# Performance work log

Hardware: AMD Instinct MI355X
Metric: run time of the kernel (lower is better)

Reference implementation:

```python
import jax, jax.numpy as jnp
import numpy as np

N = 10000      # nodes
E = 160000     # edges
B = 16         # graphs in batch
F_NODE = 42
F_EDGE = 12
D = 256        # hidden_dim
H = 4          # heads
C = D // H     # per-head channels = 64
L = 5          # num_layers
NEG_SLOPE = 0.2  # GATConv leaky_relu slope


def layernorm(x, g, b, eps=1e-5):
    mu = jnp.mean(x, axis=-1, keepdims=True)
    var = jnp.var(x, axis=-1, keepdims=True)
    return (x - mu) * jax.lax.rsqrt(var + eps) * g + b


def setup_inputs() -> dict:
    key = jax.random.key(0)
    ks = jax.random.split(key, 20)
    def w(i, shape, scale=0.05):
        return jax.random.normal(ks[i], shape, dtype=jnp.float32) * scale
    return {
        "x": jax.random.normal(ks[0], (N, F_NODE), dtype=jnp.float32),
        "edge_attr": jax.random.normal(ks[1], (E, F_EDGE), dtype=jnp.float32),
        "edge_index": jax.random.randint(ks[2], (2, E), 0, N),
        "batch": jnp.sort(jax.random.randint(ks[3], (N,), 0, B)),
        # node / edge encoders
        "enc_w": w(4, (F_NODE, D)), "enc_b": jnp.zeros((D,), jnp.float32),
        "eenc_w": w(5, (F_EDGE, D)), "eenc_b": jnp.zeros((D,), jnp.float32),
        # stacked GAT layer params [L, ...]
        "gat_w": w(6, (L, D, D)),          # lin_src == lin_dst (shared in PyG for Tensor input)
        "att_src": w(7, (L, H, C)),
        "att_dst": w(8, (L, H, C)),
        "att_edge": w(9, (L, H, C)),
        "gat_ew": w(10, (L, D, D)),        # lin_edge
        "gat_b": jnp.zeros((L, D), jnp.float32),
        "ln_g": jnp.ones((L, D), jnp.float32),
        "ln_b": jnp.zeros((L, D), jnp.float32),
        # attention pooling gate MLP
        "gate_w1": w(11, (D, D)), "gate_b1": jnp.zeros((D,), jnp.float32),
        "gate_w2": w(12, (D, 1)), "gate_b2": jnp.zeros((1,), jnp.float32),
        # MLP readout (mlp_layers=2)
        "ro_w1": w(13, (D, D)), "ro_b1": jnp.zeros((D,), jnp.float32),
        "ro_w2": w(14, (D, D)), "ro_b2": jnp.zeros((D,), jnp.float32),
    }


def reference(x, edge_index, edge_attr, batch, enc_w, enc_b, eenc_w, eenc_b,
              gat_w, att_src, att_dst, att_edge, gat_ew, gat_b, ln_g, ln_b,
              gate_w1, gate_b1, gate_w2, gate_b2, ro_w1, ro_b1, ro_w2, ro_b2):
    src0, dst0 = edge_index[0], edge_index[1]

    # encoders (dropout is identity at eval)
    h = jax.nn.relu(x @ enc_w + enc_b)                      # [N, D]
    e = jax.nn.relu(edge_attr @ eenc_w + eenc_b)            # [E, D]

    # GATConv add_self_loops with fill_value='mean': self-loop edge feature is
    # the mean of incoming edge features per destination node.
    esum = jax.ops.segment_sum(e, dst0, num_segments=N)
    cnt = jax.ops.segment_sum(jnp.ones((E,), e.dtype), dst0, num_segments=N)
    e_self = esum / jnp.maximum(cnt, 1.0)[:, None]
    e_full = jnp.concatenate([e, e_self], axis=0)           # [E+N, D]
    loops = jnp.arange(N)
    src = jnp.concatenate([src0, loops])
    dst = jnp.concatenate([dst0, loops])

    for l in range(L):
        xh = (h @ gat_w[l]).reshape(N, H, C)                # [N, H, C]
        a_s = jnp.einsum('nhc,hc->nh', xh, att_src[l])      # [N, H]
        a_d = jnp.einsum('nhc,hc->nh', xh, att_dst[l])
        eh = (e_full @ gat_ew[l]).reshape(-1, H, C)         # [E+N, H, C]
        a_e = jnp.einsum('ehc,hc->eh', eh, att_edge[l])
        alpha = jax.nn.leaky_relu(a_s[src] + a_d[dst] + a_e, NEG_SLOPE)  # [E+N, H]
        # softmax over incoming edges per destination node (stable)
        m = jax.lax.stop_gradient(jax.ops.segment_max(alpha, dst, num_segments=N))
        ex = jnp.exp(alpha - m[dst])
        den = jax.ops.segment_sum(ex, dst, num_segments=N)
        attn = ex / den[dst]                                # [E+N, H]
        msg = xh[src] * attn[:, :, None]                    # [E+N, H, C]
        out = jax.ops.segment_sum(msg, dst, num_segments=N).reshape(N, D) + gat_b[l]
        out = jax.nn.relu(layernorm(out, ln_g[l], ln_b[l]))
        h = h + out                                         # residual

    # GlobalAttention pooling: softmax(gate_nn(h)) per graph, weighted sum
    gate = (jax.nn.relu(h @ gate_w1 + gate_b1) @ gate_w2 + gate_b2)[:, 0]  # [N]
    gm = jax.lax.stop_gradient(jax.ops.segment_max(gate, batch, num_segments=B))
    ge = jnp.exp(gate - gm[batch])
    gd = jax.ops.segment_sum(ge, batch, num_segments=B)
    wgt = ge / gd[batch]
    g_embed = jax.ops.segment_sum(h * wgt[:, None], batch, num_segments=B)  # [B, D]

    # MLP readout
    return jax.nn.relu(g_embed @ ro_w1 + ro_b1) @ ro_w2 + ro_b2  # [B, D]
```

## Files before the change

kernel.cpp:

```cpp
#include <hip/hip_runtime.h>
#include <math.h>

#define DD 256
#define HH 4
#define CC 64
#define LL 5
#define NEG_SLOPE 0.2f
#define LH 20
#define WCAP 192

typedef __bf16 bf16x8 __attribute__((ext_vector_type(8)));
typedef __bf16 bf16x4 __attribute__((ext_vector_type(4)));
typedef float f32x4 __attribute__((ext_vector_type(4)));

static __device__ __forceinline__ float lrelu(float x) {
    return x > 0.0f ? x : NEG_SLOPE * x;
}

__global__ __launch_bounds__(256) void mega_setup_kernel(
    const float* __restrict__ gat_ew, const float* __restrict__ att_edge,
    float* __restrict__ wproj,
    const float* __restrict__ gat_w, const float* __restrict__ gate_w1,
    __bf16* __restrict__ wf,
    const int* __restrict__ dst_arr, int* __restrict__ deg,
    const float* __restrict__ x, const float* __restrict__ enc_w,
    const float* __restrict__ enc_b, float* __restrict__ h,
    __bf16* __restrict__ hbf,
    float* __restrict__ g_embed, float* __restrict__ gate_out,
    int N, int E, int B) {
    int blk = blockIdx.x;
    int tid = threadIdx.x;
    int EB = (E + 255) >> 8;
    if (blk < 5) {
        int l = blk;
        int k = tid;
        const float* W = gat_ew + (size_t)l * DD * DD;
        const float* att = att_edge + l * DD;
        for (int hh = 0; hh < HH; ++hh) {
            float s = 0.f;
            #pragma unroll
            for (int c = 0; c < CC; ++c)
                s += W[k * DD + hh * CC + c] * att[hh * CC + c];
            wproj[k * LH + l * HH + hh] = s;
        }
        return;
    }
    blk -= 5;
    if (blk < 192) {
        int b = blk;
        int l = b >> 5;
        int rem = b & 31;
        int y = rem >> 3, ks = rem & 7;
        int t = tid >> 6, lane = tid & 63;
        int q = lane >> 4, r15 = lane & 15;
        const float* W = (l < 5) ? (gat_w + (size_t)l * DD * DD) : gate_w1;
        size_t obase = (((size_t)b * 4 + t) * 64 + lane) * 8;
        int kbase = ks * 32 + q * 8;
        int col = y * 64 + t * 16 + r15;
        #pragma unroll
        for (int j = 0; j < 8; ++j)
            wf[obase + j] = (__bf16)W[(size_t)(kbase + j) * DD + col];
        return;
    }
    blk -= 192;
    if (blk < EB) {
        int e = blk * 256 + tid;
        if (e < E) atomicAdd(&deg[dst_arr[e]], 1);
        return;
    }
    blk -= EB;
    if (blk < N) {
        int n = blk;
        __shared__ float xs[42];
        if (tid < 42) xs[tid] = x[(size_t)n * 42 + tid];
        __syncthreads();
        float acc = enc_b[tid];
        #pragma unroll
        for (int f = 0; f < 42; ++f) acc += xs[f] * enc_w[f * DD + tid];
        float v = fmaxf(acc, 0.f);
        h[(size_t)n * DD + tid] = v;
        hbf[(size_t)n * DD + tid] = (__bf16)v;
        return;
    }
    blk -= N;
    if (blk == 0) {
        for (int i = tid; i < B * DD; i += 256) g_embed[i] = 0.f;
        return;
    }
    for (int i = tid; i < N; i += 256) gate_out[i] = 0.f;
}

__global__ __launch_bounds__(1024) void scan_pack_kernel(
    const int* __restrict__ deg, int* __restrict__ row_ptr,
    int* __restrict__ cursor, int n,
    const float* __restrict__ eenc_w, const float* __restrict__ eenc_b,
    const float* __restrict__ wproj, __bf16* __restrict__ wfe,
    __bf16* __restrict__ wfp) {
    int tid = threadIdx.x;
    if (blockIdx.x == 1) {
        {
            int idx = tid;
            int t = idx >> 6, lane = idx & 63;
            int q = lane >> 4, r15 = lane & 15;
            int col = t * 16 + r15;
            #pragma unroll
            for (int j = 0; j < 8; ++j) {
                int k = q * 8 + j;
                float v = (k < 12) ? eenc_w[k * 256 + col]
                                   : (k == 12 ? eenc_b[col] : 0.f);
                wfe[(size_t)idx * 8 + j] = (__bf16)v;
            }
        }
        {
            int idx = tid;
            int sidx = idx >> 6, lane = idx & 63;
            int s = sidx >> 1, t2 = sidx & 1;
            int q = lane >> 4, r15 = lane & 15;
            int col = t2 * 16 + r15;
            #pragma unroll
            for (int j = 0; j < 8; ++j) {
                int k = s * 32 + q * 8 + j;
                float v = (col < LH) ? wproj[k * LH + col] : 0.f;
                wfp[(size_t)idx * 8 + j] = (__bf16)v;
            }
        }
        return;
    }
    __shared__ int wsum[16];
    __shared__ int carry_s;
    int w = tid >> 6, lane = tid & 63;
    if (tid == 0) carry_s = 0;
    __syncthreads();
    for (int base = 0; base < n; base += 1024) {
        int i = base + tid;
        int v = (i < n) ? deg[i] : 0;
        int carry = carry_s;
        int s = v;
        #pragma unroll
        for (int off = 1; off < 64; off <<= 1) {
            int t = __shfl_up(s, off, 64);
            if (lane >= off) s += t;
        }
        if (lane == 63) wsum[w] = s;
        __syncthreads();
        if (w == 0 && lane < 16) {
            int ws = wsum[lane];
            #pragma unroll
            for (int off = 1; off < 16; off <<= 1) {
                int t = __shfl_up(ws, off, 64);
                if (lane >= off) ws += t;
            }
            wsum[lane] = ws;
        }
        __syncthreads();
        int waveoff = (w == 0) ? 0 : wsum[w - 1];
        if (i < n) {
            int ex = carry + waveoff + s - v;
            row_ptr[i] = ex;
            cursor[i] = ex;
        }
        __syncthreads();
        if (tid == 0) carry_s = carry + wsum[15];
        __syncthreads();
    }
    if (tid == 0) row_ptr[n] = carry_s;
}

__global__ __launch_bounds__(256) void edge_mfma_kernel(
    const float* __restrict__ edge_attr, const __bf16* __restrict__ wfe,
    const __bf16* __restrict__ wfp,
    const int* __restrict__ src_arr, const int* __restrict__ dst_arr,
    int* __restrict__ cursor, int* __restrict__ csr_src,
    float* __restrict__ a_e, int E, int N) {
    __shared__ __bf16 sm[4][16][264];
    __shared__ int pkbuf[4][16];
    int tid = threadIdx.x;
    int w = tid >> 6, lane = tid & 63;
    int q = lane >> 4, r15 = lane & 15;
    int eb = blockIdx.x * 64 + w * 16;
    int e = eb + r15;
    int ec = min(e, E - 1);
    if (q == 0 && e < E) {
        int d = dst_arr[e];
        int pk = atomicAdd(&cursor[d], 1);
        csr_src[pk] = src_arr[e];
        pkbuf[w][r15] = pk;
    }
    bf16x8 a1;
    #pragma unroll
    for (int j = 0; j < 8; ++j) a1[j] = (__bf16)0.f;
    if (q == 0) {
        const float4* p = (const float4*)(edge_attr + (size_t)ec * 12);
        float4 p0 = p[0], p1 = p[1];
        a1[0] = (__bf16)p0.x; a1[1] = (__bf16)p0.y; a1[2] = (__bf16)p0.z; a1[3] = (__bf16)p0.w;
        a1[4] = (__bf16)p1.x; a1[5] = (__bf16)p1.y; a1[6] = (__bf16)p1.z; a1[7] = (__bf16)p1.w;
    } else if (q == 1) {
        float4 p2 = *(const float4*)(edge_attr + (size_t)ec * 12 + 8);
        a1[0] = (__bf16)p2.x; a1[1] = (__bf16)p2.y; a1[2] = (__bf16)p2.z; a1[3] = (__bf16)p2.w;
        a1[4] = (__bf16)1.0f;
    }
    const bf16x8* wfeP = (const bf16x8*)wfe;
    f32x4 zero = (f32x4){0.f, 0.f, 0.f, 0.f};
    #pragma unroll
    for (int t = 0; t < 16; ++t) {
        bf16x8 bfr = wfeP[t * 64 + lane];
        f32x4 c = __builtin_amdgcn_mfma_f32_16x16x32_bf16(a1, bfr, zero, 0, 0, 0);
        int col = t * 16 + r15;
        #pragma unroll
        for (int r = 0; r < 4; ++r)
            sm[w][q * 4 + r][col] = (__bf16)fmaxf(c[r], 0.f);
    }
    const bf16x8* wfpP = (const bf16x8*)wfp;
    f32x4 c2[2];
    c2[0] = zero; c2[1] = zero;
    #pragma unroll
    for (int s = 0; s < 8; ++s) {
        bf16x8 a2 = *(const bf16x8*)&sm[w][r15][s * 32 + q * 8];
        #pragma unroll
        for (int t2 = 0; t2 < 2; ++t2)
            c2[t2] = __builtin_amdgcn_mfma_f32_16x16x32_bf16(
                a2, wfpP[(s * 2 + t2) * 64 + lane], c2[t2], 0, 0, 0);
    }
    size_t stride_l = (size_t)(E + N) * 4;
    #pragma unroll
    for (int t2 = 0; t2 < 2; ++t2) {
        int col = t2 * 16 + r15;
        if (col >= LH) continue;
        int l = col >> 2, hh = col & 3;
        #pragma unroll
        for (int r = 0; r < 4; ++r) {
            int e2 = eb + q * 4 + r;
            if (e2 < E) {
                int pk = pkbuf[w][q * 4 + r];
                a_e[(size_t)l * stride_l + (size_t)pk * 4 + hh] = c2[t2][r];
            }
        }
    }
}

__global__ void self_ae_kernel(const int* __restrict__ row_ptr,
                               float* __restrict__ a_e, int N, int E) {
    int i = blockIdx.x * 256 + threadIdx.x;
    if (i >= N * LH) return;
    int n = i / LH;
    int j = i % LH;
    int l = j >> 2, hh = j & 3;
    int rs = row_ptr[n], re = row_ptr[n + 1];
    size_t base = (size_t)l * (size_t)(E + N) * 4;
    float s = 0.f;
    for (int k = rs; k < re; ++k)
        s += a_e[base + (size_t)k * 4 + hh];
    a_e[base + (size_t)(E + n) * 4 + hh] = s / (float)max(re - rs, 1);
}

__global__ __launch_bounds__(256) void gemm_mfma_kernel(
    const __bf16* __restrict__ hbf, const __bf16* __restrict__ wf,
    __bf16* __restrict__ xhbf, int M,
    const float* __restrict__ att_src, const float* __restrict__ att_dst,
    float* __restrict__ a_s, float* __restrict__ a_d,
    const float* __restrict__ bias, const float* __restrict__ gate_w2,
    const float* __restrict__ gate_b2, float* __restrict__ gate_out) {
    int tid = threadIdx.x;
    int w = tid >> 6, lane = tid & 63;
    int q = lane >> 4, r15 = lane & 15;
    int m0 = blockIdx.x * 64;
    int y2 = blockIdx.y;
    int arow = m0 + w * 16 + r15;
    int arowc = min(arow, M - 1);
    const __bf16* ap = hbf + (size_t)arowc * DD + q * 8;
    const bf16x8* wfP = (const bf16x8*)wf;
    f32x4 acc[8];
    #pragma unroll
    for (int g = 0; g < 8; ++g) acc[g] = (f32x4){0.f, 0.f, 0.f, 0.f};
    #pragma unroll
    for (int ks = 0; ks < 8; ++ks) {
        bf16x8 a = *(const bf16x8*)(ap + ks * 32);
        #pragma unroll
        for (int g = 0; g < 8; ++g) {
            int y = y2 * 2 + (g >> 2);
            int t = g & 3;
            bf16x8 b = wfP[(size_t)(((y * 8 + ks) * 4) + t) * 64 + lane];
            acc[g] = __builtin_amdgcn_mfma_f32_16x16x32_bf16(a, b, acc[g], 0, 0, 0);
        }
    }
    if (xhbf) {
        #pragma unroll
        for (int g = 0; g < 8; ++g) {
            int col = (y2 * 8 + g) * 16 + r15;
            #pragma unroll
            for (int r = 0; r < 4; ++r) {
                int rc = m0 + w * 16 + q * 4 + r;
                if (rc < M) xhbf[(size_t)rc * DD + col] = (__bf16)acc[g][r];
            }
        }
    }
    if (att_src) {
        #pragma unroll
        for (int r = 0; r < 4; ++r) {
            float ps0 = 0.f, pd0 = 0.f, ps1 = 0.f, pd1 = 0.f;
            #pragma unroll
            for (int g = 0; g < 8; ++g) {
                int col = (y2 * 8 + g) * 16 + r15;
                float v = acc[g][r];
                if (g < 4) { ps0 += v * att_src[col]; pd0 += v * att_dst[col]; }
                else       { ps1 += v * att_src[col]; pd1 += v * att_dst[col]; }
            }
            #pragma unroll
            for (int mask = 1; mask < 16; mask <<= 1) {
                ps0 += __shfl_xor(ps0, mask, 64);
                pd0 += __shfl_xor(pd0, mask, 64);
                ps1 += __shfl_xor(ps1, mask, 64);
                pd1 += __shfl_xor(pd1, mask, 64);
            }
            int rc = m0 + w * 16 + q * 4 + r;
            if (r15 == 0 && rc < M) {
                a_s[rc * HH + y2 * 2 + 0] = ps0;
                a_d[rc * HH + y2 * 2 + 0] = pd0;
                a_s[rc * HH + y2 * 2 + 1] = ps1;
                a_d[rc * HH + y2 * 2 + 1] = pd1;
            }
        }
    }
    if (gate_w2) {
        #pragma unroll
        for (int r = 0; r < 4; ++r) {
            float pg = 0.f;
            #pragma unroll
            for (int g = 0; g < 8; ++g) {
                int col = (y2 * 8 + g) * 16 + r15;
                pg += fmaxf(acc[g][r] + bias[col], 0.f) * gate_w2[col];
            }
            #pragma unroll
            for (int mask = 1; mask < 16; mask <<= 1) pg += __shfl_xor(pg, mask, 64);
            int rc = m0 + w * 16 + q * 4 + r;
            if (r15 == 0 && rc < M) {
                float add = pg + (y2 == 0 ? gate_b2[0] : 0.f);
                atomicAdd(&gate_out[rc], add);
            }
        }
    }
}

__global__ __launch_bounds__(256) void gat_message8_kernel(
    const __bf16* __restrict__ xhbf, const float* __restrict__ a_s,
    const float* __restrict__ a_d, const float* __restrict__ a_e,
    const int* __restrict__ row_ptr, const int* __restrict__ csr_src,
    const float* __restrict__ gat_b,
    const float* __restrict__ ln_g, const float* __restrict__ ln_b,
    float* __restrict__ h, __bf16* __restrict__ hbf, int N, int E) {
    __shared__ float lws[4][WCAP * 4];
    __shared__ int lsrc[4][WCAP];
    int tid = threadIdx.x;
    int w = tid >> 6, lane = tid & 63;
    int n = blockIdx.x * 4 + w;
    if (n >= N) return;
    int hh = lane >> 4, j = lane & 15;
    int rs = row_ptr[n], re = row_ptr[n + 1];
    int deg = re - rs;
    float adn = a_d[n * HH + hh];
    float al_self = lrelu(a_s[n * HH + hh] + adn + a_e[(size_t)(E + n) * 4 + hh]);
    float m = al_self, den = 0.f;
    for (int k = rs + j; k < re; k += 16) {
        int kk = k - rs;
        int s = csr_src[k];
        float a = lrelu(a_s[s * HH + hh] + adn + a_e[(size_t)k * 4 + hh]);
        if (kk < WCAP) {
            lws[w][kk * 4 + hh] = a;
            if (hh == 0) lsrc[w][kk] = s;
        }
        float mn = fmaxf(m, a);
        den = den * __expf(m - mn) + __expf(a - mn);
        m = mn;
    }
    #pragma unroll
    for (int off = 1; off < 16; off <<= 1) {
        float m2 = __shfl_xor(m, off, 64);
        float d2 = __shfl_xor(den, off, 64);
        float mn = fmaxf(m, m2);
        den = den * __expf(m - mn) + d2 * __expf(m2 - mn);
        m = mn;
    }
    den += __expf(al_self - m);
    float inv_den = 1.0f / den;
    int cap = min(deg, WCAP);
    for (int kk = j; kk < cap; kk += 16)
        lws[w][kk * 4 + hh] = __expf(lws[w][kk * 4 + hh] - m) * inv_den;
    float wself = __expf(al_self - m) * inv_den;
    bf16x4 xsb = *((const bf16x4*)(xhbf + (size_t)n * DD) + lane);
    float4 acc;
    acc.x = wself * (float)xsb[0]; acc.y = wself * (float)xsb[1];
    acc.z = wself * (float)xsb[2]; acc.w = wself * (float)xsb[3];
    if (deg <= WCAP) {
        int k = rs;
        for (; k + 3 < re; k += 4) {
            int kk = k - rs;
            int s0 = lsrc[w][kk + 0], s1_ = lsrc[w][kk + 1];
            int s2_ = lsrc[w][kk + 2], s3_ = lsrc[w][kk + 3];
            float w0 = lws[w][(kk + 0) * 4 + hh], w1 = lws[w][(kk + 1) * 4 + hh];
            float w2 = lws[w][(kk + 2) * 4 + hh], w3 = lws[w][(kk + 3) * 4 + hh];
            bf16x4 x0 = *((const bf16x4*)(xhbf + (size_t)s0 * DD) + lane);
            bf16x4 x1 = *((const bf16x4*)(xhbf + (size_t)s1_ * DD) + lane);
            bf16x4 x2 = *((const bf16x4*)(xhbf + (size_t)s2_ * DD) + lane);
            bf16x4 x3 = *((const bf16x4*)(xhbf + (size_t)s3_ * DD) + lane);
            acc.x += w0 * (float)x0[0] + w1 * (float)x1[0] + w2 * (float)x2[0] + w3 * (float)x3[0];
            acc.y += w0 * (float)x0[1] + w1 * (float)x1[1] + w2 * (float)x2[1] + w3 * (float)x3[1];
            acc.z += w0 * (float)x0[2] + w1 * (float)x1[2] + w2 * (float)x2[2] + w3 * (float)x3[2];
            acc.w += w0 * (float)x0[3] + w1 * (float)x1[3] + w2 * (float)x2[3] + w3 * (float)x3[3];
        }
        for (; k < re; ++k) {
            int kk = k - rs;
            int s0 = lsrc[w][kk];
            float w0 = lws[w][kk * 4 + hh];
            bf16x4 x0 = *((const bf16x4*)(xhbf + (size_t)s0 * DD) + lane);
            acc.x += w0 * (float)x0[0]; acc.y += w0 * (float)x0[1];
            acc.z += w0 * (float)x0[2]; acc.w += w0 * (float)x0[3];
        }
    } else {
        for (int k = rs; k < re; ++k) {
            int kk = k - rs;
            int s0;
            float w0;
            if (kk < WCAP) { s0 = lsrc[w][kk]; w0 = lws[w][kk * 4 + hh]; }
            else {
                s0 = csr_src[k];
                w0 = __expf(lrelu(a_s[s0 * HH + hh] + adn + a_e[(size_t)k * 4 + hh]) - m) * inv_den;
            }
            bf16x4 x0 = *((const bf16x4*)(xhbf + (size_t)s0 * DD) + lane);
            acc.x += w0 * (float)x0[0]; acc.y += w0 * (float)x0[1];
            acc.z += w0 * (float)x0[2]; acc.w += w0 * (float)x0[3];
        }
    }
    float4 gb = *((const float4*)gat_b + lane);
    float4 val;
    val.x = acc.x + gb.x; val.y = acc.y + gb.y;
    val.z = acc.z + gb.z; val.w = acc.w + gb.w;
    float s1 = val.x + val.y + val.z + val.w;
    float s2 = val.x * val.x + val.y * val.y + val.z * val.z + val.w * val.w;
    #pragma unroll
    for (int off = 1; off < 64; off <<= 1) {
        s1 += __shfl_xor(s1, off, 64);
        s2 += __shfl_xor(s2, off, 64);
    }
    float mu = s1 * (1.0f / DD);
    float var = s2 * (1.0f / DD) - mu * mu;
    float rstd = rsqrtf(var + 1e-5f);
    float4 lg = *((const float4*)ln_g + lane);
    float4 lb = *((const float4*)ln_b + lane);
    float4 nv;
    nv.x = fmaxf((val.x - mu) * rstd * lg.x + lb.x, 0.f);
    nv.y = fmaxf((val.y - mu) * rstd * lg.y + lb.y, 0.f);
    nv.z = fmaxf((val.z - mu) * rstd * lg.z + lb.z, 0.f);
    nv.w = fmaxf((val.w - mu) * rstd * lg.w + lb.w, 0.f);
    float4* hp = (float4*)(h + (size_t)n * DD) + lane;
    float4 hv = *hp;
    hv.x += nv.x; hv.y += nv.y; hv.z += nv.z; hv.w += nv.w;
    *hp = hv;
    bf16x4 hb;
    hb[0] = (__bf16)hv.x; hb[1] = (__bf16)hv.y;
    hb[2] = (__bf16)hv.z; hb[3] = (__bf16)hv.w;
    *((bf16x4*)(hbf + (size_t)n * DD) + lane) = hb;
}

__global__ __launch_bounds__(256) void gseg_kernel(
    const float* __restrict__ gate, const int* __restrict__ batch,
    float* __restrict__ gmax, float* __restrict__ gden, int N) {
    int b = blockIdx.x;
    int tid = threadIdx.x;
    __shared__ int bounds[2];
    if (tid < 2) {
        int target = b + tid;
        int lo = 0, hi = N;
        while (lo < hi) {
            int mid = (lo + hi) >> 1;
            if (batch[mid] < target) lo = mid + 1; else hi = mid;
        }
        bounds[tid] = lo;
    }
    __syncthreads();
    int s0 = bounds[0], s1 = bounds[1];
    __shared__ float red[256];
    float m = -1e30f;
    for (int i = s0 + tid; i < s1; i += 256) m = fmaxf(m, gate[i]);
    red[tid] = m;
    __syncthreads();
    for (int off = 128; off; off >>= 1) {
        if (tid < off) red[tid] = fmaxf(red[tid], red[tid + off]);
        __syncthreads();
    }
    float gm = red[0];
    __syncthreads();
    float s = 0.f;
    for (int i = s0 + tid; i < s1; i += 256) s += __expf(gate[i] - gm);
    red[tid] = s;
    __syncthreads();
    for (int off = 128; off; off >>= 1) {
        if (tid < off) red[tid] += red[tid + off];
        __syncthreads();
    }
    if (tid == 0) {
        gmax[b] = gm;
        gden[b] = red[0];
    }
}

#define POOL_CHUNK 32
__global__ __launch_bounds__(256) void pool_scatter_kernel(
    const float* __restrict__ h, const float* __restrict__ gate,
    const float* __restrict__ gmax, const float* __restrict__ gden,
    const int* __restrict__ batch, float* __restrict__ g_embed, int N) {
    int i0 = blockIdx.x * POOL_CHUNK;
    int d = threadIdx.x;
    int iend = min(i0 + POOL_CHUNK, N);
    float acc = 0.f;
    int cur = batch[i0];
    for (int i = i0; i < iend; ++i) {
        int b = batch[i];
        if (b != cur) {
            atomicAdd(&g_embed[cur * DD + d], acc);
            acc = 0.f;
            cur = b;
        }
        float wgt = __expf(gate[i] - gmax[b]) / gden[b];
        acc += wgt * h[(size_t)i * DD + d];
    }
    atomicAdd(&g_embed[cur * DD + d], acc);
}

__global__ __launch_bounds__(256) void readout_kernel(
    const float* __restrict__ g_embed, const float* __restrict__ w1,
    const float* __restrict__ b1, const float* __restrict__ w2,
    const float* __restrict__ b2, float* __restrict__ out) {
    int b = blockIdx.x;
    int tid = threadIdx.x;
    __shared__ float gvec[256];
    __shared__ float hid[256];
    gvec[tid] = g_embed[b * DD + tid];
    __syncthreads();
    float hv = b1[tid];
    for (int k = 0; k < DD; ++k) hv += gvec[k] * w1[k * DD + tid];
    hid[tid] = fmaxf(hv, 0.f);
    __syncthreads();
    float o = b2[tid];
    for (int t = 0; t < DD; ++t) o += hid[t] * w2[t * DD + tid];
    out[b * DD + tid] = o;
}

extern "C" void kernel_launch(void* const* d_in, const int* in_sizes, int n_in,
                              void* d_out, int out_size, void* d_ws, size_t ws_size,
                              hipStream_t stream) {
    const float* x        = (const float*)d_in[0];
    const float* edge_attr= (const float*)d_in[1];
    const int*   edge_idx = (const int*)d_in[2];
    const int*   batch    = (const int*)d_in[3];
    const float* enc_w    = (const float*)d_in[4];
    const float* enc_b    = (const float*)d_in[5];
    const float* eenc_w   = (const float*)d_in[6];
    const float* eenc_b   = (const float*)d_in[7];
    const float* gat_w    = (const float*)d_in[8];
    const float* att_src  = (const float*)d_in[9];
    const float* att_dst  = (const float*)d_in[10];
    const float* att_edge = (const float*)d_in[11];
    const float* gat_ew   = (const float*)d_in[12];
    const float* gat_b    = (const float*)d_in[13];
    const float* ln_g     = (const float*)d_in[14];
    const float* ln_b     = (const float*)d_in[15];
    const float* gate_w1  = (const float*)d_in[16];
    const float* gate_b1  = (const float*)d_in[17];
    const float* gate_w2  = (const float*)d_in[18];
    const float* gate_b2  = (const float*)d_in[19];
    const float* ro_w1    = (const float*)d_in[20];
    const float* ro_b1    = (const float*)d_in[21];
    const float* ro_w2    = (const float*)d_in[22];
    const float* ro_b2    = (const float*)d_in[23];
    float* out = (float*)d_out;

    const int N = in_sizes[0] / 42;
    const int E = in_sizes[1] / 12;
    const int B = out_size / DD;

    char* p = (char*)d_ws;
    auto alloc = [&](size_t bytes) {
        char* r = p;
        p += (bytes + 255) & ~(size_t)255;
        return (void*)r;
    };
    float*  h       = (float*)alloc((size_t)N * DD * 4);
    __bf16* hbf     = (__bf16*)alloc((size_t)N * DD * 2);
    __bf16* xhbf    = (__bf16*)alloc((size_t)N * DD * 2);
    float*  a_s     = (float*)alloc((size_t)N * HH * 4);
    float*  a_d     = (float*)alloc((size_t)N * HH * 4);
    float*  a_e_csr = (float*)alloc((size_t)LL * (E + N) * 4 * 4);
    float*  wproj   = (float*)alloc((size_t)DD * LH * 4);
    __bf16* wfe     = (__bf16*)alloc((size_t)16 * 64 * 8 * 2);
    __bf16* wfp     = (__bf16*)alloc((size_t)16 * 64 * 8 * 2);
    __bf16* wf      = (__bf16*)alloc((size_t)6 * DD * DD * 2);
    float*  gate    = (float*)alloc((size_t)N * 4);
    float*  g_embed = (float*)alloc((size_t)B * DD * 4);
    float*  gmax    = (float*)alloc((size_t)B * 4);
    float*  gden    = (float*)alloc((size_t)B * 4);
    int* deg        = (int*)alloc((size_t)N * 4);
    int* row_ptr    = (int*)alloc((size_t)(N + 1) * 4);
    int* cursor     = (int*)alloc((size_t)N * 4);
    int* csr_src    = (int*)alloc((size_t)E * 4);

    const int* src_arr = edge_idx;
    const int* dst_arr = edge_idx + E;

    hipMemsetAsync(deg, 0, (size_t)N * 4, stream);

    const int EB = (E + 255) / 256;
    int mega_grid = 5 + 192 + EB + N + 2;
    mega_setup_kernel<<<mega_grid, 256, 0, stream>>>(
        gat_ew, att_edge, wproj, gat_w, gate_w1, wf,
        dst_arr, deg, x, enc_w, enc_b, h, hbf, g_embed, gate, N, E, B);
    scan_pack_kernel<<<2, 1024, 0, stream>>>(
        deg, row_ptr, cursor, N, eenc_w, eenc_b, wproj, wfe, wfp);
    edge_mfma_kernel<<<(E + 63) / 64, 256, 0, stream>>>(
        edge_attr, wfe, wfp, src_arr, dst_arr, cursor, csr_src, a_e_csr, E, N);
    self_ae_kernel<<<(N * LH + 255) / 256, 256, 0, stream>>>(
        row_ptr, a_e_csr, N, E);

    dim3 ggrid((N + 63) / 64, 2);
    size_t lstride = (size_t)(E + N) * 4;
    for (int l = 0; l < LL; ++l) {
        gemm_mfma_kernel<<<ggrid, 256, 0, stream>>>(
            hbf, wf + (size_t)l * DD * DD, xhbf, N,
            att_src + l * DD, att_dst + l * DD, a_s, a_d,
            nullptr, nullptr, nullptr, nullptr);
        gat_message8_kernel<<<(N + 3) / 4, 256, 0, stream>>>(
            xhbf, a_s, a_d, a_e_csr + (size_t)l * lstride, row_ptr, csr_src,
            gat_b + l * DD, ln_g + l * DD, ln_b + l * DD, h, hbf, N, E);
    }

    gemm_mfma_kernel<<<ggrid, 256, 0, stream>>>(
        hbf, wf + (size_t)5 * DD * DD, nullptr, N,
        nullptr, nullptr, nullptr, nullptr,
        gate_b1, gate_w2, gate_b2, gate);
    gseg_kernel<<<B, 256, 0, stream>>>(gate, batch, gmax, gden, N);
    pool_scatter_kernel<<<(N + POOL_CHUNK - 1) / POOL_CHUNK, 256, 0, stream>>>(
        h, gate, gmax, gden, batch, g_embed, N);
    readout_kernel<<<B, 256, 0, stream>>>(g_embed, ro_w1, ro_b1, ro_w2, ro_b2, out);
}
```

Measured before the change: 376.4 us.

## Move node encoder to MFMA inside edge kernel and store edge attention logits as bf16

The per-node scalar encoder (one block per node in the setup kernel) is replaced by an MFMA-based encoder. It runs as extra blocks of the edge MFMA kernel, using a bf16 fragment-packed enc_w with the bias folded in as row 42. Separately, the precomputed per-edge attention logits a_e are stored as bf16 instead of fp32, halving their traffic in self_ae and in every layer's message kernel. This gives up some precision in the encoder output and the attention logits.

```diff
diff --git a/kernel.cpp b/kernel.cpp
--- a/kernel.cpp
+++ b/kernel.cpp
@@ -23,9 +23,8 @@
     const float* __restrict__ gat_w, const float* __restrict__ gate_w1,
     __bf16* __restrict__ wf,
     const int* __restrict__ dst_arr, int* __restrict__ deg,
-    const float* __restrict__ x, const float* __restrict__ enc_w,
-    const float* __restrict__ enc_b, float* __restrict__ h,
-    __bf16* __restrict__ hbf,
+    const float* __restrict__ enc_w, const float* __restrict__ enc_b,
+    __bf16* __restrict__ wfenc,
     float* __restrict__ g_embed, float* __restrict__ gate_out,
     int N, int E, int B) {
     int blk = blockIdx.x;
@@ -69,25 +68,27 @@
         return;
     }
     blk -= EB;
-    if (blk < N) {
-        int n = blk;
-        __shared__ float xs[42];
-        if (tid < 42) xs[tid] = x[(size_t)n * 42 + tid];
-        __syncthreads();
-        float acc = enc_b[tid];
-        #pragma unroll
-        for (int f = 0; f < 42; ++f) acc += xs[f] * enc_w[f * DD + tid];
-        float v = fmaxf(acc, 0.f);
-        h[(size_t)n * DD + tid] = v;
-        hbf[(size_t)n * DD + tid] = (__bf16)v;
-        return;
-    }
-    blk -= N;
     if (blk == 0) {
         for (int i = tid; i < B * DD; i += 256) g_embed[i] = 0.f;
         return;
     }
-    for (int i = tid; i < N; i += 256) gate_out[i] = 0.f;
+    if (blk == 1) {
+        for (int i = tid; i < N; i += 256) gate_out[i] = 0.f;
+        return;
+    }
+    for (int idx = tid; idx < 2 * 16 * 64; idx += 256) {
+        int ks = idx >> 10;
+        int rem = idx & 1023;
+        int t = rem >> 6, lane = rem & 63;
+        int q = lane >> 4, r15 = lane & 15;
+        int col = t * 16 + r15;
+        #pragma unroll
+        for (int j = 0; j < 8; ++j) {
+            int k = ks * 32 + q * 8 + j;
+            float v = (k < 42) ? enc_w[k * DD + col] : (k == 42 ? enc_b[col] : 0.f);
+            wfenc[(size_t)idx * 8 + j] = (__bf16)v;
+        }
+    }
 }
 
 __global__ __launch_bounds__(1024) void scan_pack_kernel(
@@ -166,17 +167,57 @@
     if (tid == 0) row_ptr[n] = carry_s;
 }
 
-__global__ __launch_bounds__(256) void edge_mfma_kernel(
+__global__ __launch_bounds__(256) void edge_enc_mfma_kernel(
     const float* __restrict__ edge_attr, const __bf16* __restrict__ wfe,
     const __bf16* __restrict__ wfp,
     const int* __restrict__ src_arr, const int* __restrict__ dst_arr,
     int* __restrict__ cursor, int* __restrict__ csr_src,
-    float* __restrict__ a_e, int E, int N) {
+    __bf16* __restrict__ a_e,
+    const float* __restrict__ x, const __bf16* __restrict__ wfenc,
+    float* __restrict__ h, __bf16* __restrict__ hbf,
+    int E, int N) {
     __shared__ __bf16 sm[4][16][264];
     __shared__ int pkbuf[4][16];
     int tid = threadIdx.x;
     int w = tid >> 6, lane = tid & 63;
     int q = lane >> 4, r15 = lane & 15;
+    int EBLK = (E + 63) >> 6;
+    f32x4 zero = (f32x4){0.f, 0.f, 0.f, 0.f};
+    if (blockIdx.x >= EBLK) {
+        int nb = (blockIdx.x - EBLK) * 64 + w * 16;
+        if (nb >= N) return;
+        int n = min(nb + r15, N - 1);
+        bf16x8 aA[2];
+        #pragma unroll
+        for (int ks = 0; ks < 2; ++ks) {
+            #pragma unroll
+            for (int j = 0; j < 8; ++j) {
+                int k = ks * 32 + q * 8 + j;
+                float v = (k < 42) ? x[(size_t)n * 42 + k] : (k == 42 ? 1.0f : 0.f);
+                aA[ks][j] = (__bf16)v;
+            }
+        }
+        const bf16x8* wp = (const bf16x8*)wfenc;
+        #pragma unroll
+        for (int t = 0; t < 16; ++t) {
+            f32x4 c = zero;
+            #pragma unroll
+            for (int ks = 0; ks < 2; ++ks)
+                c = __builtin_amdgcn_mfma_f32_16x16x32_bf16(
+                    aA[ks], wp[(ks * 16 + t) * 64 + lane], c, 0, 0, 0);
+            int col = t * 16 + r15;
+            #pragma unroll
+            for (int r = 0; r < 4; ++r) {
+                int n2 = nb + q * 4 + r;
+                if (n2 < N) {
+                    float v = fmaxf(c[r], 0.f);
+                    h[(size_t)n2 * DD + col] = v;
+                    hbf[(size_t)n2 * DD + col] = (__bf16)v;
+                }
+            }
+        }
+        return;
+    }
     int eb = blockIdx.x * 64 + w * 16;
     int e = eb + r15;
     int ec = min(e, E - 1);
@@ -200,7 +241,6 @@
         a1[4] = (__bf16)1.0f;
     }
     const bf16x8* wfeP = (const bf16x8*)wfe;
-    f32x4 zero = (f32x4){0.f, 0.f, 0.f, 0.f};
     #pragma unroll
     for (int t = 0; t < 16; ++t) {
         bf16x8 bfr = wfeP[t * 64 + lane];
@@ -232,14 +272,14 @@
             int e2 = eb + q * 4 + r;
             if (e2 < E) {
                 int pk = pkbuf[w][q * 4 + r];
-                a_e[(size_t)l * stride_l + (size_t)pk * 4 + hh] = c2[t2][r];
+                a_e[(size_t)l * stride_l + (size_t)pk * 4 + hh] = (__bf16)c2[t2][r];
             }
         }
     }
 }
 
 __global__ void self_ae_kernel(const int* __restrict__ row_ptr,
-                               float* __restrict__ a_e, int N, int E) {
+                               __bf16* __restrict__ a_e, int N, int E) {
     int i = blockIdx.x * 256 + threadIdx.x;
     if (i >= N * LH) return;
     int n = i / LH;
@@ -249,8 +289,8 @@
     size_t base = (size_t)l * (size_t)(E + N) * 4;
     float s = 0.f;
     for (int k = rs; k < re; ++k)
-        s += a_e[base + (size_t)k * 4 + hh];
-    a_e[base + (size_t)(E + n) * 4 + hh] = s / (float)max(re - rs, 1);
+        s += (float)a_e[base + (size_t)k * 4 + hh];
+    a_e[base + (size_t)(E + n) * 4 + hh] = (__bf16)(s / (float)max(re - rs, 1));
 }
 
 __global__ __launch_bounds__(256) void gemm_mfma_kernel(
@@ -341,9 +381,9 @@
     }
 }
 
-__global__ __launch_bounds__(256) void gat_message8_kernel(
+__global__ __launch_bounds__(256) void gat_message9_kernel(
     const __bf16* __restrict__ xhbf, const float* __restrict__ a_s,
-    const float* __restrict__ a_d, const float* __restrict__ a_e,
+    const float* __restrict__ a_d, const __bf16* __restrict__ a_e,
     const int* __restrict__ row_ptr, const int* __restrict__ csr_src,
     const float* __restrict__ gat_b,
     const float* __restrict__ ln_g, const float* __restrict__ ln_b,
@@ -358,12 +398,12 @@
     int rs = row_ptr[n], re = row_ptr[n + 1];
     int deg = re - rs;
     float adn = a_d[n * HH + hh];
-    float al_self = lrelu(a_s[n * HH + hh] + adn + a_e[(size_t)(E + n) * 4 + hh]);
+    float al_self = lrelu(a_s[n * HH + hh] + adn + (float)a_e[(size_t)(E + n) * 4 + hh]);
     float m = al_self, den = 0.f;
     for (int k = rs + j; k < re; k += 16) {
         int kk = k - rs;
         int s = csr_src[k];
-        float a = lrelu(a_s[s * HH + hh] + adn + a_e[(size_t)k * 4 + hh]);
+        float a = lrelu(a_s[s * HH + hh] + adn + (float)a_e[(size_t)k * 4 + hh]);
         if (kk < WCAP) {
             lws[w][kk * 4 + hh] = a;
             if (hh == 0) lsrc[w][kk] = s;
@@ -423,7 +463,7 @@
             if (kk < WCAP) { s0 = lsrc[w][kk]; w0 = lws[w][kk * 4 + hh]; }
             else {
                 s0 = csr_src[k];
-                w0 = __expf(lrelu(a_s[s0 * HH + hh] + adn + a_e[(size_t)k * 4 + hh]) - m) * inv_den;
+                w0 = __expf(lrelu(a_s[s0 * HH + hh] + adn + (float)a_e[(size_t)k * 4 + hh]) - m) * inv_den;
             }
             bf16x4 x0 = *((const bf16x4*)(xhbf + (size_t)s0 * DD) + lane);
             acc.x += w0 * (float)x0[0]; acc.y += w0 * (float)x0[1];
@@ -589,10 +629,11 @@
     __bf16* xhbf    = (__bf16*)alloc((size_t)N * DD * 2);
     float*  a_s     = (float*)alloc((size_t)N * HH * 4);
     float*  a_d     = (float*)alloc((size_t)N * HH * 4);
-    float*  a_e_csr = (float*)alloc((size_t)LL * (E + N) * 4 * 4);
+    __bf16* a_e_csr = (__bf16*)alloc((size_t)LL * (E + N) * 4 * 2);
     float*  wproj   = (float*)alloc((size_t)DD * LH * 4);
     __bf16* wfe     = (__bf16*)alloc((size_t)16 * 64 * 8 * 2);
     __bf16* wfp     = (__bf16*)alloc((size_t)16 * 64 * 8 * 2);
+    __bf16* wfenc   = (__bf16*)alloc((size_t)2 * 16 * 64 * 8 * 2);
     __bf16* wf      = (__bf16*)alloc((size_t)6 * DD * DD * 2);
     float*  gate    = (float*)alloc((size_t)N * 4);
     float*  g_embed = (float*)alloc((size_t)B * DD * 4);
@@ -609,14 +650,17 @@
     hipMemsetAsync(deg, 0, (size_t)N * 4, stream);
 
     const int EB = (E + 255) / 256;
-    int mega_grid = 5 + 192 + EB + N + 2;
+    int mega_grid = 5 + 192 + EB + 3;
     mega_setup_kernel<<<mega_grid, 256, 0, stream>>>(
         gat_ew, att_edge, wproj, gat_w, gate_w1, wf,
-        dst_arr, deg, x, enc_w, enc_b, h, hbf, g_embed, gate, N, E, B);
+        dst_arr, deg, enc_w, enc_b, wfenc, g_embed, gate, N, E, B);
     scan_pack_kernel<<<2, 1024, 0, stream>>>(
         deg, row_ptr, cursor, N, eenc_w, eenc_b, wproj, wfe, wfp);
-    edge_mfma_kernel<<<(E + 63) / 64, 256, 0, stream>>>(
-        edge_attr, wfe, wfp, src_arr, dst_arr, cursor, csr_src, a_e_csr, E, N);
+    const int EBLK = (E + 63) / 64;
+    const int NBLK = (N + 63) / 64;
+    edge_enc_mfma_kernel<<<EBLK + NBLK, 256, 0, stream>>>(
+        edge_attr, wfe, wfp, src_arr, dst_arr, cursor, csr_src, a_e_csr,
+        x, wfenc, h, hbf, E, N);
     self_ae_kernel<<<(N * LH + 255) / 256, 256, 0, stream>>>(
         row_ptr, a_e_csr, N, E);
 
@@ -627,7 +671,7 @@
             hbf, wf + (size_t)l * DD * DD, xhbf, N,
             att_src + l * DD, att_dst + l * DD, a_s, a_d,
             nullptr, nullptr, nullptr, nullptr);
-        gat_message8_kernel<<<(N + 3) / 4, 256, 0, stream>>>(
+        gat_message9_kernel<<<(N + 3) / 4, 256, 0, stream>>>(
             xhbf, a_s, a_d, a_e_csr + (size_t)l * lstride, row_ptr, csr_src,
             gat_b + l * DD, ln_g + l * DD, ln_b + l * DD, h, hbf, N, E);
     }
```

Result: no change. 380.3 us (+1.0%).
